# Kernel tuning notes

Measured on AMD Instinct MI355X. Metric: run time of the kernel, lower is better.

## Reference

```python
import jax, jax.numpy as jnp
import numpy as np

S, O, H = 8, 1024, 1024
B, N = 32, 512

def setup_inputs() -> dict:
    key = jax.random.key(0)
    k1, k2, k3, k4 = jax.random.split(key, 4)
    x = jax.random.normal(k1, (B, N, H), dtype=jnp.float32)
    subject_id = jax.random.randint(k2, (B,), 0, S)
    # kaiming_uniform_(a=sqrt(5)) on [S,O,H]: fan_in=H, gain=sqrt(2/(1+5)), bound=gain*sqrt(3/fan_in)
    wbound = jnp.sqrt(2.0 / 6.0) * jnp.sqrt(3.0 / H)
    weight = jax.random.uniform(k3, (S, O, H), minval=-wbound, maxval=wbound, dtype=jnp.float32)
    bbound = 1.0 / jnp.sqrt(H)
    bias = jax.random.uniform(k4, (S, O), minval=-bbound, maxval=bbound, dtype=jnp.float32)
    return {"x": x, "subject_id": subject_id, "weight": weight, "bias": bias}

def reference(x, subject_id, weight, bias):
    # Per-sample weight gather + batched matmul + bias add
    W = weight[subject_id]          # [B, O, H]
    b = bias[subject_id]            # [B, O]
    y = jnp.einsum('bnh,boh->bno', x, W) + b[:, None, :]
    return y
```

## Files before the change

kernel.cpp:

```cpp
#include <hip/hip_runtime.h>


constexpr int S_DIM = 8;
constexpr int O_DIM = 1024;
constexpr int H_DIM = 1024;
constexpr int B_DIM = 32;
constexpr int N_DIM = 512;

constexpr int BM = 256;
constexpr int BN = 256;
constexpr int BK = 64;
constexpr int NKT = H_DIM / BK;

constexpr long long X_ELEMS = (long long)B_DIM * N_DIM * H_DIM;
constexpr size_t XB_BYTES = (size_t)X_ELEMS * 2;

typedef short bf16x8 __attribute__((ext_vector_type(8)));
typedef float f32x4 __attribute__((ext_vector_type(4)));
typedef float f32x2 __attribute__((ext_vector_type(2)));
typedef __bf16 bf16x2 __attribute__((ext_vector_type(2)));

__device__ __forceinline__ unsigned int cvt_pk_bf16(float a, float b) {
  f32x2 v;
  v[0] = a;
  v[1] = b;
  bf16x2 r = __builtin_convertvector(v, bf16x2);
  return __builtin_bit_cast(unsigned int, r);
}

__device__ __forceinline__ void gload_lds16(const void* g, void* l) {
  __builtin_amdgcn_global_load_lds(
      (const __attribute__((address_space(1))) unsigned int*)g,
      (__attribute__((address_space(3))) unsigned int*)l, 16, 0, 0);
}

__global__ __launch_bounds__(256) void cvt_kernel(
    const float* __restrict__ x, const float* __restrict__ w,
    unsigned short* __restrict__ xb, unsigned short* __restrict__ wb) {
  const int blk = blockIdx.x;
  const float* src;
  unsigned short* dst;
  long long base;
  if (blk < 4096) {
    src = x; dst = xb; base = (long long)blk * 4096;
  } else {
    src = w; dst = wb; base = (long long)(blk - 4096) * 4096;
  }
  const long long e0 = base + threadIdx.x * 4;
#pragma unroll
  for (int c = 0; c < 4; ++c) {
    const f32x4 v = __builtin_nontemporal_load((const f32x4*)(src + e0 + c * 1024));
    uint2 u;
    u.x = cvt_pk_bf16(v[0], v[1]);
    u.y = cvt_pk_bf16(v[2], v[3]);
    *(uint2*)(dst + e0 + c * 1024) = u;
  }
}

#define BAR() __builtin_amdgcn_s_barrier()
#define VMW(N) asm volatile("s_waitcnt vmcnt(" #N ")" ::: "memory")
#define LGKM0()                                            \
  do {                                                     \
    asm volatile("s_waitcnt lgkmcnt(0)" ::: "memory");     \
    __builtin_amdgcn_sched_barrier(0);                     \
  } while (0)

#define LDA4(ABUF, MB)                                                   \
  do {                                                                   \
    _Pragma("unroll") for (int m_ = 0; m_ < 4; ++m_) {                   \
      const int ar_ = wr * 128 + ((MB) + m_) * 16 + lcol;                \
      const unsigned short* ap_ = (ABUF) + ar_ * BK;                     \
      af[m_][0] = *(const bf16x8*)(ap_ + (pc0 << 3));                    \
      af[m_][1] = *(const bf16x8*)(ap_ + ((pc0 ^ 4) << 3));              \
    }                                                                    \
  } while (0)

#define LDB2(BBUF, NB)                                                   \
  do {                                                                   \
    _Pragma("unroll") for (int n_ = 0; n_ < 2; ++n_) {                   \
      const int br_ = wc * 64 + ((NB) + n_) * 16 + lcol;                 \
      const unsigned short* bp_ = (BBUF) + br_ * BK;                     \
      bfr[n_][0] = *(const bf16x8*)(bp_ + (pc0 << 3));                   \
      bfr[n_][1] = *(const bf16x8*)(bp_ + ((pc0 ^ 4) << 3));             \
    }                                                                    \
  } while (0)

#define MM4(MB, NB)                                                         \
  do {                                                                      \
    _Pragma("unroll") for (int m_ = 0; m_ < 4; ++m_)                        \
    _Pragma("unroll") for (int n_ = 0; n_ < 2; ++n_)                        \
    _Pragma("unroll") for (int x_ = 0; x_ < 2; ++x_)                        \
      acc[(MB) + m_][(NB) + n_] = __builtin_amdgcn_mfma_f32_16x16x32_bf16(  \
          af[m_][x_], bfr[n_][x_], acc[(MB) + m_][(NB) + n_], 0, 0, 0);     \
  } while (0)

#define STAGE_A(H, DST, KT)                                                 \
  do {                                                                      \
    gload_lds16(agA + (size_t)((H) * 64) * H_DIM + (KT) * 64,               \
                (DST) + ((H) * 64 + wid * 8) * BK);                         \
    gload_lds16(agA + (size_t)((H) * 64 + 128) * H_DIM + (KT) * 64,         \
                (DST) + ((H) * 64 + 128 + wid * 8) * BK);                   \
  } while (0)

#define STAGE_B(S, DST, KT)                                                 \
  do {                                                                      \
    gload_lds16(bgB0 + (size_t)((S) * 32) * H_DIM + (KT) * 64,              \
                (DST) + (bq0 + (S) * 32) * BK);                             \
    gload_lds16(bgB1 + (size_t)((S) * 32) * H_DIM + (KT) * 64,              \
                (DST) + (bq1 + (S) * 32) * BK);                             \
  } while (0)

__global__ __launch_bounds__(512, 2) void scl_gemm(
    const unsigned short* __restrict__ xb, const int* __restrict__ subject_id,
    const unsigned short* __restrict__ wb, const float* __restrict__ bias,
    float* __restrict__ out) {
  __shared__ __align__(16) unsigned short As[2][BM * BK];
  __shared__ __align__(16) unsigned short Bs[2][BN * BK];

  const int tid = threadIdx.x;
  const int lane = tid & 63;
  const int wid = tid >> 6;
  const int wr = wid >> 2;
  const int wc = wid & 3;
  const int lcol = lane & 15;
  const int lq = lane >> 4;
  const int rl = lane >> 3;
  const int pc0 = lq ^ (lane & 7);

  const int bid = blockIdx.x;
  const int b = (bid & 7) * 4 + ((bid >> 3) & 3);
  const int t = bid >> 5;
  const int n0 = (t & 1) * BM;
  const int o0 = (t >> 1) * BN;
  const int sid = subject_id[b];

  const int skc = ((lane & 7) ^ rl) << 3;
  const unsigned short* agA =
      xb + (size_t)(b * N_DIM + n0 + wid * 8 + rl) * H_DIM + skc;
  const int bq0 = ((wid * 2) >> 2) * 64 + ((wid * 2) & 3) * 8;
  const int bq1 = ((wid * 2 + 1) >> 2) * 64 + ((wid * 2 + 1) & 3) * 8;
  const unsigned short* bgB0 =
      wb + (size_t)(sid * O_DIM + o0 + bq0 + rl) * H_DIM + skc;
  const unsigned short* bgB1 =
      wb + (size_t)(sid * O_DIM + o0 + bq1 + rl) * H_DIM + skc;

  unsigned short* const As0 = &As[0][0];
  unsigned short* const As1 = &As[1][0];
  unsigned short* const Bs0 = &Bs[0][0];
  unsigned short* const Bs1 = &Bs[1][0];

  f32x4 acc[8][4];
#pragma unroll
  for (int mi = 0; mi < 8; ++mi)
#pragma unroll
    for (int ni = 0; ni < 4; ++ni) {
      f32x4 z = {0.f, 0.f, 0.f, 0.f};
      acc[mi][ni] = z;
    }

  bf16x8 af[4][2];
  bfr_decl:;
  bf16x8 bfr[2][2];

  STAGE_A(0, As0, 0);
  STAGE_B(0, Bs0, 0);
  STAGE_A(1, As0, 0);
  STAGE_B(1, Bs0, 0);
  STAGE_A(0, As1, 1);
  STAGE_B(0, Bs1, 1);
  VMW(8);
  BAR();

#pragma unroll
  for (int kt = 0; kt < NKT; ++kt) {
    unsigned short* const Ac = (kt & 1) ? As1 : As0;
    unsigned short* const Bc = (kt & 1) ? Bs1 : Bs0;
    unsigned short* const Ao = (kt & 1) ? As0 : As1;
    unsigned short* const Bo = (kt & 1) ? Bs0 : Bs1;

    LDA4(Ac, 0);
    LDB2(Bc, 0);
    if (kt + 1 < NKT) {
      STAGE_A(1, Ao, kt + 1);
      VMW(6);
    } else {
      VMW(0);
    }
    BAR();
    LGKM0();
    __builtin_amdgcn_s_setprio(1);
    MM4(0, 0);
    __builtin_amdgcn_s_setprio(0);
    BAR();

    LDB2(Bc, 2);
    if (kt + 1 < NKT) STAGE_B(1, Bo, kt + 1);
    BAR();
    LGKM0();
    __builtin_amdgcn_s_setprio(1);
    MM4(0, 2);
    __builtin_amdgcn_s_setprio(0);
    BAR();

    LDA4(Ac, 4);
    LDB2(Bc, 0);
    if (kt + 2 < NKT) STAGE_A(0, Ac, kt + 2);
    BAR();
    LGKM0();
    __builtin_amdgcn_s_setprio(1);
    MM4(4, 0);
    __builtin_amdgcn_s_setprio(0);
    BAR();

    LDB2(Bc, 2);
    if (kt + 2 < NKT) {
      STAGE_B(0, Bc, kt + 2);
      VMW(8);
    } else if (kt + 2 == NKT) {
      VMW(4);
    }
    BAR();
    LGKM0();
    __builtin_amdgcn_s_setprio(1);
    MM4(4, 2);
    __builtin_amdgcn_s_setprio(0);
    BAR();
  }

  float bv[4];
#pragma unroll
  for (int ni = 0; ni < 4; ++ni)
    bv[ni] = bias[sid * O_DIM + o0 + wc * 64 + ni * 16 + lcol];

  float* outb =
      out + (size_t)(b * N_DIM + n0 + wr * 128) * O_DIM + o0 + wc * 64 + lcol;
#pragma unroll
  for (int mi = 0; mi < 8; ++mi) {
#pragma unroll
    for (int r = 0; r < 4; ++r) {
      float* orow = outb + (size_t)(mi * 16 + lq * 4 + r) * O_DIM;
#pragma unroll
      for (int ni = 0; ni < 4; ++ni)
        orow[ni * 16] = acc[mi][ni][r] + bv[ni];
    }
  }
}

extern "C" void kernel_launch(void* const* d_in, const int* in_sizes, int n_in,
                              void* d_out, int out_size, void* d_ws, size_t ws_size,
                              hipStream_t stream) {
  const float* x = (const float*)d_in[0];
  const int* subject_id = (const int*)d_in[1];
  const float* weight = (const float*)d_in[2];
  const float* bias = (const float*)d_in[3];
  float* out = (float*)d_out;

  unsigned short* xb = (unsigned short*)d_ws;
  unsigned short* wb = (unsigned short*)((char*)d_ws + XB_BYTES);

  cvt_kernel<<<6144, 256, 0, stream>>>(x, weight, xb, wb);

  scl_gemm<<<256, 512, 0, stream>>>(xb, subject_id, wb, bias, out);
}
```

Measured before the change: 179.3 us.

## Software-pipeline LDS fragment loads behind MFMA phases with split B registers

Restructures the k-loop so each phase's LDS fragment reads for the next MFMA block are issued right after the current MFMA batch, overlapping LDS latency with compute. B fragments are split into low and high register sets so they can be reused across phases without reloading, and the loop is manually unrolled by two with explicit buffer ping-pong and unroll 1. The aim is to remove exposed LDS wait time before each MFMA block and cut redundant LDS reads. In exchange it needs more registers and much more careful vmcnt and barrier accounting, which risks correctness hazards.

```diff
diff --git a/kernel.cpp b/kernel.cpp
--- a/kernel.cpp
+++ b/kernel.cpp
@@ -58,6 +58,7 @@
 }
 
 #define BAR() __builtin_amdgcn_s_barrier()
+#define SB0() __builtin_amdgcn_sched_barrier(0)
 #define VMW(N) asm volatile("s_waitcnt vmcnt(" #N ")" ::: "memory")
 #define LGKM0()                                            \
   do {                                                     \
@@ -65,33 +66,33 @@
     __builtin_amdgcn_sched_barrier(0);                     \
   } while (0)
 
-#define LDA4(ABUF, MB)                                                   \
+#define LDA4T(DST, ABUF, MB)                                             \
   do {                                                                   \
     _Pragma("unroll") for (int m_ = 0; m_ < 4; ++m_) {                   \
       const int ar_ = wr * 128 + ((MB) + m_) * 16 + lcol;                \
       const unsigned short* ap_ = (ABUF) + ar_ * BK;                     \
-      af[m_][0] = *(const bf16x8*)(ap_ + (pc0 << 3));                    \
-      af[m_][1] = *(const bf16x8*)(ap_ + ((pc0 ^ 4) << 3));              \
-    }                                                                    \
-  } while (0)
-
-#define LDB2(BBUF, NB)                                                   \
+      DST[m_][0] = *(const bf16x8*)(ap_ + (pc0 << 3));                   \
+      DST[m_][1] = *(const bf16x8*)(ap_ + ((pc0 ^ 4) << 3));             \
+    }                                                                    \
+  } while (0)
+
+#define LDB2T(DST, BBUF, NB)                                             \
   do {                                                                   \
     _Pragma("unroll") for (int n_ = 0; n_ < 2; ++n_) {                   \
       const int br_ = wc * 64 + ((NB) + n_) * 16 + lcol;                 \
       const unsigned short* bp_ = (BBUF) + br_ * BK;                     \
-      bfr[n_][0] = *(const bf16x8*)(bp_ + (pc0 << 3));                   \
-      bfr[n_][1] = *(const bf16x8*)(bp_ + ((pc0 ^ 4) << 3));             \
-    }                                                                    \
-  } while (0)
-
-#define MM4(MB, NB)                                                         \
+      DST[n_][0] = *(const bf16x8*)(bp_ + (pc0 << 3));                   \
+      DST[n_][1] = *(const bf16x8*)(bp_ + ((pc0 ^ 4) << 3));             \
+    }                                                                    \
+  } while (0)
+
+#define MM4(AF, BF, MB, NB)                                                 \
   do {                                                                      \
     _Pragma("unroll") for (int m_ = 0; m_ < 4; ++m_)                        \
     _Pragma("unroll") for (int n_ = 0; n_ < 2; ++n_)                        \
     _Pragma("unroll") for (int x_ = 0; x_ < 2; ++x_)                        \
       acc[(MB) + m_][(NB) + n_] = __builtin_amdgcn_mfma_f32_16x16x32_bf16(  \
-          af[m_][x_], bfr[n_][x_], acc[(MB) + m_][(NB) + n_], 0, 0, 0);     \
+          AF[m_][x_], BF[n_][x_], acc[(MB) + m_][(NB) + n_], 0, 0, 0);      \
   } while (0)
 
 #define STAGE_A(H, DST, KT)                                                 \
@@ -108,6 +109,55 @@
                 (DST) + (bq0 + (S) * 32) * BK);                             \
     gload_lds16(bgB1 + (size_t)((S) * 32) * H_DIM + (KT) * 64,              \
                 (DST) + (bq1 + (S) * 32) * BK);                             \
+  } while (0)
+
+#define KTILE(KT, AC, BC, AO, BO)                                        \
+  do {                                                                   \
+        \
+    LGKM0();                                                             \
+    __builtin_amdgcn_s_setprio(1);                                       \
+    MM4(af, bfL, 0, 0);                                                  \
+    __builtin_amdgcn_s_setprio(0);                                       \
+    LDB2T(bfH, BC, 2);                             \
+    if ((KT) + 1 < NKT) STAGE_A(1, AO, (KT) + 1);                        \
+    SB0();                                                               \
+    BAR();                                                               \
+                                                  \
+    LGKM0();                                                             \
+    __builtin_amdgcn_s_setprio(1);                                       \
+    MM4(af, bfH, 0, 2);                                                  \
+    __builtin_amdgcn_s_setprio(0);                                       \
+    LDA4T(af, AC, 4);                           \
+    if ((KT) + 1 < NKT) STAGE_B(1, BO, (KT) + 1);                        \
+    SB0();                                                               \
+    BAR();                                                               \
+                                                  \
+    LGKM0();                                                             \
+    __builtin_amdgcn_s_setprio(1);                                       \
+    MM4(af, bfH, 4, 2);                                                  \
+    __builtin_amdgcn_s_setprio(0);                                       \
+    if ((KT) + 2 < NKT) {                                                \
+      STAGE_A(0, AC, (KT) + 2);                                          \
+      STAGE_B(0, BC, (KT) + 2);                                          \
+      VMW(8);            \
+    } else if ((KT) + 2 == NKT) {                                        \
+      VMW(4);                                                            \
+    }                                                                    \
+    SB0();                                                               \
+    BAR();                                                               \
+                                                  \
+    LGKM0();                                                             \
+    __builtin_amdgcn_s_setprio(1);                                       \
+    MM4(af, bfL, 4, 0);                                                  \
+    __builtin_amdgcn_s_setprio(0);                                       \
+    if ((KT) + 1 < NKT) {                                                \
+      LDA4T(af, AO, 0);                                 \
+      LDB2T(bfL, BO, 0);                                \
+      if ((KT) + 2 < NKT) VMW(4);          \
+      else VMW(0);                   \
+    }                                                                    \
+    SB0();                                                               \
+    BAR();                                                               \
   } while (0)
 
 __global__ __launch_bounds__(512, 2) void scl_gemm(
@@ -159,8 +209,8 @@
     }
 
   bf16x8 af[4][2];
-  bfr_decl:;
-  bf16x8 bfr[2][2];
+  bf16x8 bfL[2][2];
+  bf16x8 bfH[2][2];
 
   STAGE_A(0, As0, 0);
   STAGE_B(0, Bs0, 0);
@@ -168,63 +218,16 @@
   STAGE_B(1, Bs0, 0);
   STAGE_A(0, As1, 1);
   STAGE_B(0, Bs1, 1);
-  VMW(8);
+  VMW(4);
   BAR();
-
-#pragma unroll
-  for (int kt = 0; kt < NKT; ++kt) {
-    unsigned short* const Ac = (kt & 1) ? As1 : As0;
-    unsigned short* const Bc = (kt & 1) ? Bs1 : Bs0;
-    unsigned short* const Ao = (kt & 1) ? As0 : As1;
-    unsigned short* const Bo = (kt & 1) ? Bs0 : Bs1;
-
-    LDA4(Ac, 0);
-    LDB2(Bc, 0);
-    if (kt + 1 < NKT) {
-      STAGE_A(1, Ao, kt + 1);
-      VMW(6);
-    } else {
-      VMW(0);
-    }
-    BAR();
-    LGKM0();
-    __builtin_amdgcn_s_setprio(1);
-    MM4(0, 0);
-    __builtin_amdgcn_s_setprio(0);
-    BAR();
-
-    LDB2(Bc, 2);
-    if (kt + 1 < NKT) STAGE_B(1, Bo, kt + 1);
-    BAR();
-    LGKM0();
-    __builtin_amdgcn_s_setprio(1);
-    MM4(0, 2);
-    __builtin_amdgcn_s_setprio(0);
-    BAR();
-
-    LDA4(Ac, 4);
-    LDB2(Bc, 0);
-    if (kt + 2 < NKT) STAGE_A(0, Ac, kt + 2);
-    BAR();
-    LGKM0();
-    __builtin_amdgcn_s_setprio(1);
-    MM4(4, 0);
-    __builtin_amdgcn_s_setprio(0);
-    BAR();
-
-    LDB2(Bc, 2);
-    if (kt + 2 < NKT) {
-      STAGE_B(0, Bc, kt + 2);
-      VMW(8);
-    } else if (kt + 2 == NKT) {
-      VMW(4);
-    }
-    BAR();
-    LGKM0();
-    __builtin_amdgcn_s_setprio(1);
-    MM4(4, 2);
-    __builtin_amdgcn_s_setprio(0);
-    BAR();
+  LDA4T(af, As0, 0);
+  LDB2T(bfL, Bs0, 0);
+  SB0();
+
+#pragma unroll 1
+  for (int kt = 0; kt < NKT; kt += 2) {
+    KTILE(kt, As0, Bs0, As1, Bs1);
+    KTILE(kt + 1, As1, Bs1, As0, Bs0);
   }
 
   float bv[4];
```

After: 177.6 us. No clear change (-0.9%).
